# Kernel tuning notes

Hardware: AMD Instinct MI355X
Metric: run time of the kernel (lower is better)

The kernel has to match this reference:

```python
import jax, jax.numpy as jnp
import numpy as np

SEQ, BS, H, I, E = 2048, 4, 2048, 4096, 8


def setup_inputs() -> dict:
    key = jax.random.key(0)
    ks = jax.random.split(key, 5)
    s = 0.02
    return {
        "hidden_states": jax.random.normal(ks[0], (SEQ, BS, H), dtype=jnp.float32),
        "router_w": jax.random.normal(ks[1], (H, E), dtype=jnp.float32) * s,
        "gate_w": jax.random.normal(ks[2], (E, H, I), dtype=jnp.float32) * s,
        "up_w": jax.random.normal(ks[3], (E, H, I), dtype=jnp.float32) * s,
        "down_w": jax.random.normal(ks[4], (E, I, H), dtype=jnp.float32) * s,
    }


def reference(hidden_states, router_w, gate_w, up_w, down_w):
    # Router: [S,B,H] @ [H,E] -> [S,B,E]; top-1 routing (num_experts_per_tok == 1)
    router_logits = jnp.einsum("sbh,he->sbe", hidden_states, router_w)
    routing_indices = jnp.argmax(router_logits, axis=-1)  # [S,B]
    # sigmoid routing weights are computed but NOT applied in the original combine
    routing_weights = jax.nn.sigmoid(jnp.max(router_logits, axis=-1))  # noqa: F841

    out = jnp.zeros_like(hidden_states)
    for e in range(E):  # small fixed expert count
        mask = (routing_indices == e)[..., None]  # [S,B,1]
        g = jnp.einsum("sbh,hi->sbi", hidden_states, gate_w[e])
        u = jnp.einsum("sbh,hi->sbi", hidden_states, up_w[e])
        y = jnp.einsum("sbi,ih->sbh", jax.nn.silu(g) * u, down_w[e])
        out = out + jnp.where(mask, y, jnp.zeros((), out.dtype))
    return out
```

## Files before the change

kernel.cpp:

```cpp
#include <hip/hip_runtime.h>
#include <hip/hip_bf16.h>

#define T_TOKENS 8192
#define H_DIM 2048
#define I_DIM 4096
#define E_EXP 8
#define PAD_ROWS 9216

typedef __bf16 bf16x8 __attribute__((ext_vector_type(8)));
typedef float floatx4 __attribute__((ext_vector_type(4)));
typedef unsigned short ushort8 __attribute__((ext_vector_type(8)));

__device__ __forceinline__ unsigned short f2bf(float f) {
  union { float f; unsigned int i; } c; c.f = f;
  unsigned int x = c.i;
  unsigned int r = x + 0x7fffu + ((x >> 16) & 1u);
  return (unsigned short)(r >> 16);
}

__device__ __forceinline__ float bf2float(unsigned short u) {
  union { unsigned int i; float f; } c; c.i = ((unsigned int)u) << 16;
  return c.f;
}

__device__ __forceinline__ void gload_lds16(const void* g, void* l) {
  __builtin_amdgcn_global_load_lds(
      (const __attribute__((address_space(1))) void*)g,
      (__attribute__((address_space(3))) void*)l, 16, 0, 0);
}

__global__ __launch_bounds__(256) void xcvt_kernel(const float* __restrict__ x,
                                                   unsigned short* __restrict__ xb,
                                                   int* __restrict__ hdr) {
  if (blockIdx.x == 0 && threadIdx.x < 32) hdr[threadIdx.x] = 0;
  int i = (blockIdx.x * 256 + threadIdx.x) * 4;
  floatx4 v = *(const floatx4*)(x + i);
  unsigned short o0 = f2bf(v[0]), o1 = f2bf(v[1]), o2 = f2bf(v[2]), o3 = f2bf(v[3]);
  ushort4 o; o.x = o0; o.y = o1; o.z = o2; o.w = o3;
  *(ushort4*)(xb + i) = o;
}

__global__ __launch_bounds__(256) void router_kernel(const float* __restrict__ x,
                                                     const float* __restrict__ rw,
                                                     int* __restrict__ idx,
                                                     int* __restrict__ hdr) {
  int lane = threadIdx.x & 63;
  int t = blockIdx.x * 4 + (threadIdx.x >> 6);
  const float* xr = x + (size_t)t * H_DIM;
  float acc[8];
#pragma unroll
  for (int e = 0; e < 8; ++e) acc[e] = 0.f;
  for (int i = lane; i < H_DIM; i += 64) {
    float h = xr[i];
    floatx4 r0 = *(const floatx4*)(rw + i * 8);
    floatx4 r1 = *(const floatx4*)(rw + i * 8 + 4);
#pragma unroll
    for (int e = 0; e < 4; ++e) { acc[e] += h * r0[e]; acc[e + 4] += h * r1[e]; }
  }
#pragma unroll
  for (int off = 32; off > 0; off >>= 1)
#pragma unroll
    for (int e = 0; e < 8; ++e) acc[e] += __shfl_xor(acc[e], off, 64);
  if (lane == 0) {
    int best = 0; float bv = acc[0];
#pragma unroll
    for (int e = 1; e < 8; ++e) if (acc[e] > bv) { bv = acc[e]; best = e; }
    idx[t] = best;
    atomicAdd(&hdr[best], 1);
  }
}

__global__ __launch_bounds__(256) void setup_kernel(int* __restrict__ hdr,
                                                    int* __restrict__ rows) {
  if (threadIdx.x == 0) {
    int b = 0;
    for (int e = 0; e < 8; ++e) {
      hdr[16 + e] = b;
      b += ((hdr[e] + 127) >> 7) << 7;
    }
  }
  for (int i = threadIdx.x; i < PAD_ROWS; i += 256) rows[i] = -1;
}

__global__ __launch_bounds__(256) void scatter_kernel(const int* __restrict__ idx,
                                                      int* __restrict__ hdr,
                                                      int* __restrict__ rows) {
  int t = blockIdx.x * 256 + threadIdx.x;
  int e = idx[t];
  int p = atomicAdd(&hdr[8 + e], 1);
  rows[hdr[16 + e] + p] = t;
}

template <int K, int N>
__global__ __launch_bounds__(256) void wtrans_kernel(const float* __restrict__ W,
                                                     unsigned short* __restrict__ Wt) {
  __shared__ unsigned short tile[64 * 64];
  const int e = blockIdx.z;
  const int bn = blockIdx.x * 64;
  const int bk = blockIdx.y * 64;
  const float* Wp = W + (size_t)e * K * N;
  unsigned short* Wtp = Wt + (size_t)e * N * K;
  const int tid = threadIdx.x;

  {
    const int k = tid >> 2;
    const int n0 = (tid & 3) * 16;
    const float* src = Wp + (size_t)(bk + k) * N + bn + n0;
    floatx4 v0 = *(const floatx4*)(src);
    floatx4 v1 = *(const floatx4*)(src + 4);
    floatx4 v2 = *(const floatx4*)(src + 8);
    floatx4 v3 = *(const floatx4*)(src + 12);
    ushort8 p0, p1;
#pragma unroll
    for (int i = 0; i < 4; ++i) {
      p0[i] = f2bf(v0[i]); p0[4 + i] = f2bf(v1[i]);
      p1[i] = f2bf(v2[i]); p1[4 + i] = f2bf(v3[i]);
    }
    const int s0 = (tid & 3) * 2;
    *(ushort8*)(tile + k * 64 + ((s0 ^ (k & 7)) << 3)) = p0;
    *(ushort8*)(tile + k * 64 + (((s0 + 1) ^ (k & 7)) << 3)) = p1;
  }
  __syncthreads();
  {
    const int n = tid & 63;
    const int wv = tid >> 6;
    const int nhi = n >> 3, nlo = n & 7;
    ushort8 o0, o1;
#pragma unroll
    for (int i = 0; i < 8; ++i) {
      const int k0 = wv * 16 + i;
      const int k1 = k0 + 8;
      o0[i] = tile[k0 * 64 + (((nhi ^ (k0 & 7)) << 3) | nlo)];
      o1[i] = tile[k1 * 64 + (((nhi ^ (k1 & 7)) << 3) | nlo)];
    }
    unsigned short* dst = Wtp + (size_t)(bn + n) * K + bk + wv * 16;
    *(ushort8*)(dst) = o0;
    *(ushort8*)(dst + 8) = o1;
  }
}

template <int K, int NTOT, bool GATHER, int MODE>
__global__ __launch_bounds__(256) void moe_gemm(const unsigned short* __restrict__ A,
                                                const unsigned short* __restrict__ Bt,
                                                const int* __restrict__ hdr,
                                                const int* __restrict__ rows,
                                                unsigned short* __restrict__ gtmp,
                                                unsigned short* __restrict__ inter,
                                                float* __restrict__ outp) {
  const int e = blockIdx.z;
  const int cnt = hdr[e];
  if ((int)blockIdx.y * 128 >= cnt) return;
  const int seg = hdr[16 + e];

  const int tid = threadIdx.x;
  const int lane = tid & 63;
  const int wv = tid >> 6;
  const int wm = (wv & 1) * 64;
  const int wn = (wv >> 1) * 64;
  const int q = lane >> 4;
  const int l15 = lane & 15;

  __shared__ unsigned short sA[128 * 64];
  __shared__ unsigned short sB[128 * 64];

  const int lr = lane >> 3;
  const int colsw = (lane & 7) ^ lr;
  const unsigned short* aptr[4];
  const unsigned short* bptr[4];
  const unsigned short* Be = Bt + (size_t)e * NTOT * K;
#pragma unroll
  for (int j = 0; j < 4; ++j) {
    const int R = j * 32 + wv * 8 + lr;
    int ar;
    if (GATHER) {
      ar = rows[seg + blockIdx.y * 128 + R];
      if (ar < 0) ar = 0;
    } else {
      ar = seg + blockIdx.y * 128 + R;
    }
    aptr[j] = A + (size_t)ar * K + colsw * 8;
    bptr[j] = Be + (size_t)(blockIdx.x * 128 + R) * K + colsw * 8;
  }

  floatx4 acc[4][4];
#pragma unroll
  for (int a = 0; a < 4; ++a)
#pragma unroll
    for (int b = 0; b < 4; ++b) acc[a][b] = (floatx4){0.f, 0.f, 0.f, 0.f};

  for (int kt = 0; kt < K; kt += 64) {
#pragma unroll
    for (int j = 0; j < 4; ++j) {
      gload_lds16(aptr[j] + kt, sA + (j * 32 + wv * 8) * 64);
      gload_lds16(bptr[j] + kt, sB + (j * 32 + wv * 8) * 64);
    }
    __syncthreads();
#pragma unroll
    for (int ks = 0; ks < 64; ks += 32) {
      const int sbase = ks >> 3;
      bf16x8 af[4], bfr[4];
#pragma unroll
      for (int fm = 0; fm < 4; ++fm) {
        const int ra = wm + fm * 16 + l15;
        af[fm] = __builtin_bit_cast(bf16x8,
            *(const ushort8*)(sA + ra * 64 + (((q + sbase) ^ (ra & 7)) << 3)));
      }
#pragma unroll
      for (int fn = 0; fn < 4; ++fn) {
        const int rb = wn + fn * 16 + l15;
        bfr[fn] = __builtin_bit_cast(bf16x8,
            *(const ushort8*)(sB + rb * 64 + (((q + sbase) ^ (rb & 7)) << 3)));
      }
#pragma unroll
      for (int fm = 0; fm < 4; ++fm)
#pragma unroll
        for (int fn = 0; fn < 4; ++fn)
          acc[fm][fn] = __builtin_amdgcn_mfma_f32_16x16x32_bf16(af[fm], bfr[fn],
                                                                acc[fm][fn], 0, 0, 0);
    }
    __syncthreads();
  }

#pragma unroll
  for (int fm = 0; fm < 4; ++fm)
#pragma unroll
    for (int fn = 0; fn < 4; ++fn)
#pragma unroll
      for (int rr = 0; rr < 4; ++rr) {
        const int row = wm + fm * 16 + q * 4 + rr;
        const int col = wn + fn * 16 + l15;
        const int gm = blockIdx.y * 128 + row;
        const int gn = blockIdx.x * 128 + col;
        const float v = acc[fm][fn][rr];
        const size_t pos = (size_t)(seg + gm);
        if (MODE == 0) {
          gtmp[pos * NTOT + gn] = f2bf(v);
        } else if (MODE == 1) {
          const float g = bf2float(gtmp[pos * NTOT + gn]);
          const float s = g / (1.f + __expf(-g));
          inter[pos * NTOT + gn] = f2bf(s * v);
        } else {
          const int tok = rows[pos];
          if (tok >= 0) outp[(size_t)tok * NTOT + gn] = v;
        }
      }
}

extern "C" void kernel_launch(void* const* d_in, const int* in_sizes, int n_in,
                              void* d_out, int out_size, void* d_ws, size_t ws_size,
                              hipStream_t stream) {
  const float* hidden   = (const float*)d_in[0];
  const float* router_w = (const float*)d_in[1];
  const float* gate_w   = (const float*)d_in[2];
  const float* up_w     = (const float*)d_in[3];
  const float* down_w   = (const float*)d_in[4];
  float* out = (float*)d_out;

  char* ws = (char*)d_ws;
  int* hdr  = (int*)ws;
  int* idx  = (int*)(ws + 1024);
  int* rows = (int*)(ws + 33792);
  unsigned short* x_bf  = (unsigned short*)(ws + 70656);
  unsigned short* g_tmp = (unsigned short*)(ws + 33625088);
  unsigned short* W1    = (unsigned short*)(ws + 109122560);
  unsigned short* W2    = (unsigned short*)(ws + 243340288);
  unsigned short* inter = W1;
  unsigned short* downt = W2;

  xcvt_kernel<<<T_TOKENS * H_DIM / 1024, 256, 0, stream>>>(hidden, x_bf, hdr);
  router_kernel<<<T_TOKENS / 4, 256, 0, stream>>>(hidden, router_w, idx, hdr);
  setup_kernel<<<1, 256, 0, stream>>>(hdr, rows);
  scatter_kernel<<<T_TOKENS / 256, 256, 0, stream>>>(idx, hdr, rows);

  wtrans_kernel<H_DIM, I_DIM><<<dim3(I_DIM / 64, H_DIM / 64, E_EXP), 256, 0, stream>>>(gate_w, W1);
  wtrans_kernel<H_DIM, I_DIM><<<dim3(I_DIM / 64, H_DIM / 64, E_EXP), 256, 0, stream>>>(up_w, W2);

  moe_gemm<H_DIM, I_DIM, true, 0><<<dim3(I_DIM / 128, 64, E_EXP), 256, 0, stream>>>(
      x_bf, W1, hdr, rows, g_tmp, nullptr, nullptr);
  moe_gemm<H_DIM, I_DIM, true, 1><<<dim3(I_DIM / 128, 64, E_EXP), 256, 0, stream>>>(
      x_bf, W2, hdr, rows, g_tmp, inter, nullptr);

  wtrans_kernel<I_DIM, H_DIM><<<dim3(H_DIM / 64, I_DIM / 64, E_EXP), 256, 0, stream>>>(down_w, downt);
  moe_gemm<I_DIM, H_DIM, false, 2><<<dim3(H_DIM / 128, 64, E_EXP), 256, 0, stream>>>(
      inter, downt, hdr, rows, nullptr, nullptr, out);
}
```

Measured before the change: 1.684 ms.

## Fuse gate and up GEMMs into one kernel and rewrite weight transpose

Merges the gate and up projection GEMMs into a single kernel. It loads the gathered activation tile once, keeps two accumulator sets, and applies SiLU·up in the epilogue, so the bf16 gate intermediate no longer goes through memory. The weight transpose kernel now does register-only 8x8 transposes over 256-wide tiles instead of staging through LDS. Costs are higher register and LDS pressure in the fused kernel (launch_bounds 256,2), and the transpose writes are strided 16-byte stores.

```diff
diff --git a/kernel.cpp b/kernel.cpp
--- a/kernel.cpp
+++ b/kernel.cpp
@@ -94,59 +94,39 @@
 template <int K, int N>
 __global__ __launch_bounds__(256) void wtrans_kernel(const float* __restrict__ W,
                                                      unsigned short* __restrict__ Wt) {
-  __shared__ unsigned short tile[64 * 64];
   const int e = blockIdx.z;
-  const int bn = blockIdx.x * 64;
+  const int bn = blockIdx.x * 256;
   const int bk = blockIdx.y * 64;
   const float* Wp = W + (size_t)e * K * N;
   unsigned short* Wtp = Wt + (size_t)e * N * K;
   const int tid = threadIdx.x;
-
-  {
-    const int k = tid >> 2;
-    const int n0 = (tid & 3) * 16;
-    const float* src = Wp + (size_t)(bk + k) * N + bn + n0;
-    floatx4 v0 = *(const floatx4*)(src);
-    floatx4 v1 = *(const floatx4*)(src + 4);
-    floatx4 v2 = *(const floatx4*)(src + 8);
-    floatx4 v3 = *(const floatx4*)(src + 12);
-    ushort8 p0, p1;
-#pragma unroll
-    for (int i = 0; i < 4; ++i) {
-      p0[i] = f2bf(v0[i]); p0[4 + i] = f2bf(v1[i]);
-      p1[i] = f2bf(v2[i]); p1[4 + i] = f2bf(v3[i]);
-    }
-    const int s0 = (tid & 3) * 2;
-    *(ushort8*)(tile + k * 64 + ((s0 ^ (k & 7)) << 3)) = p0;
-    *(ushort8*)(tile + k * 64 + (((s0 + 1) ^ (k & 7)) << 3)) = p1;
-  }
-  __syncthreads();
-  {
-    const int n = tid & 63;
-    const int wv = tid >> 6;
-    const int nhi = n >> 3, nlo = n & 7;
-    ushort8 o0, o1;
-#pragma unroll
-    for (int i = 0; i < 8; ++i) {
-      const int k0 = wv * 16 + i;
-      const int k1 = k0 + 8;
-      o0[i] = tile[k0 * 64 + (((nhi ^ (k0 & 7)) << 3) | nlo)];
-      o1[i] = tile[k1 * 64 + (((nhi ^ (k1 & 7)) << 3) | nlo)];
-    }
-    unsigned short* dst = Wtp + (size_t)(bn + n) * K + bk + wv * 16;
-    *(ushort8*)(dst) = o0;
-    *(ushort8*)(dst + 8) = o1;
-  }
-}
-
-template <int K, int NTOT, bool GATHER, int MODE>
-__global__ __launch_bounds__(256) void moe_gemm(const unsigned short* __restrict__ A,
-                                                const unsigned short* __restrict__ Bt,
-                                                const int* __restrict__ hdr,
-                                                const int* __restrict__ rows,
-                                                unsigned short* __restrict__ gtmp,
-                                                unsigned short* __restrict__ inter,
-                                                float* __restrict__ outp) {
+  const int n0 = (tid & 31) * 8;
+  const int k0 = (tid >> 5) * 8;
+
+  const float* src = Wp + (size_t)(bk + k0) * N + bn + n0;
+  floatx4 a[8][2];
+#pragma unroll
+  for (int kk = 0; kk < 8; ++kk) {
+    a[kk][0] = *(const floatx4*)(src + (size_t)kk * N);
+    a[kk][1] = *(const floatx4*)(src + (size_t)kk * N + 4);
+  }
+  unsigned short* dst = Wtp + (size_t)(bn + n0) * K + bk + k0;
+#pragma unroll
+  for (int nn = 0; nn < 8; ++nn) {
+    ushort8 o;
+#pragma unroll
+    for (int kk = 0; kk < 8; ++kk) o[kk] = f2bf(a[kk][nn >> 2][nn & 3]);
+    *(ushort8*)(dst + (size_t)nn * K) = o;
+  }
+}
+
+__global__ __launch_bounds__(256, 2) void moe_gemm_gu(
+    const unsigned short* __restrict__ A,
+    const unsigned short* __restrict__ Bg,
+    const unsigned short* __restrict__ Bu,
+    const int* __restrict__ hdr,
+    const int* __restrict__ rows,
+    unsigned short* __restrict__ inter) {
   const int e = blockIdx.z;
   const int cnt = hdr[e];
   if ((int)blockIdx.y * 128 >= cnt) return;
@@ -161,38 +141,41 @@
   const int l15 = lane & 15;
 
   __shared__ unsigned short sA[128 * 64];
-  __shared__ unsigned short sB[128 * 64];
+  __shared__ unsigned short sBg[128 * 64];
+  __shared__ unsigned short sBu[128 * 64];
 
   const int lr = lane >> 3;
   const int colsw = (lane & 7) ^ lr;
   const unsigned short* aptr[4];
-  const unsigned short* bptr[4];
-  const unsigned short* Be = Bt + (size_t)e * NTOT * K;
+  const unsigned short* bgptr[4];
+  const unsigned short* buptr[4];
+  const unsigned short* BgE = Bg + (size_t)e * I_DIM * H_DIM;
+  const unsigned short* BuE = Bu + (size_t)e * I_DIM * H_DIM;
 #pragma unroll
   for (int j = 0; j < 4; ++j) {
     const int R = j * 32 + wv * 8 + lr;
-    int ar;
-    if (GATHER) {
-      ar = rows[seg + blockIdx.y * 128 + R];
-      if (ar < 0) ar = 0;
-    } else {
-      ar = seg + blockIdx.y * 128 + R;
-    }
-    aptr[j] = A + (size_t)ar * K + colsw * 8;
-    bptr[j] = Be + (size_t)(blockIdx.x * 128 + R) * K + colsw * 8;
-  }
-
-  floatx4 acc[4][4];
+    int ar = rows[seg + blockIdx.y * 128 + R];
+    if (ar < 0) ar = 0;
+    aptr[j] = A + (size_t)ar * H_DIM + colsw * 8;
+    bgptr[j] = BgE + (size_t)(blockIdx.x * 128 + R) * H_DIM + colsw * 8;
+    buptr[j] = BuE + (size_t)(blockIdx.x * 128 + R) * H_DIM + colsw * 8;
+  }
+
+  floatx4 accg[4][4], accu[4][4];
 #pragma unroll
   for (int a = 0; a < 4; ++a)
 #pragma unroll
-    for (int b = 0; b < 4; ++b) acc[a][b] = (floatx4){0.f, 0.f, 0.f, 0.f};
-
-  for (int kt = 0; kt < K; kt += 64) {
+    for (int b = 0; b < 4; ++b) {
+      accg[a][b] = (floatx4){0.f, 0.f, 0.f, 0.f};
+      accu[a][b] = (floatx4){0.f, 0.f, 0.f, 0.f};
+    }
+
+  for (int kt = 0; kt < H_DIM; kt += 64) {
 #pragma unroll
     for (int j = 0; j < 4; ++j) {
       gload_lds16(aptr[j] + kt, sA + (j * 32 + wv * 8) * 64);
-      gload_lds16(bptr[j] + kt, sB + (j * 32 + wv * 8) * 64);
+      gload_lds16(bgptr[j] + kt, sBg + (j * 32 + wv * 8) * 64);
+      gload_lds16(buptr[j] + kt, sBu + (j * 32 + wv * 8) * 64);
     }
     __syncthreads();
 #pragma unroll
@@ -209,14 +192,26 @@
       for (int fn = 0; fn < 4; ++fn) {
         const int rb = wn + fn * 16 + l15;
         bfr[fn] = __builtin_bit_cast(bf16x8,
-            *(const ushort8*)(sB + rb * 64 + (((q + sbase) ^ (rb & 7)) << 3)));
+            *(const ushort8*)(sBg + rb * 64 + (((q + sbase) ^ (rb & 7)) << 3)));
       }
 #pragma unroll
       for (int fm = 0; fm < 4; ++fm)
 #pragma unroll
         for (int fn = 0; fn < 4; ++fn)
-          acc[fm][fn] = __builtin_amdgcn_mfma_f32_16x16x32_bf16(af[fm], bfr[fn],
-                                                                acc[fm][fn], 0, 0, 0);
+          accg[fm][fn] = __builtin_amdgcn_mfma_f32_16x16x32_bf16(af[fm], bfr[fn],
+                                                                 accg[fm][fn], 0, 0, 0);
+#pragma unroll
+      for (int fn = 0; fn < 4; ++fn) {
+        const int rb = wn + fn * 16 + l15;
+        bfr[fn] = __builtin_bit_cast(bf16x8,
+            *(const ushort8*)(sBu + rb * 64 + (((q + sbase) ^ (rb & 7)) << 3)));
+      }
+#pragma unroll
+      for (int fm = 0; fm < 4; ++fm)
+#pragma unroll
+        for (int fn = 0; fn < 4; ++fn)
+          accu[fm][fn] = __builtin_amdgcn_mfma_f32_16x16x32_bf16(af[fm], bfr[fn],
+                                                                 accu[fm][fn], 0, 0, 0);
     }
     __syncthreads();
   }
@@ -231,18 +226,98 @@
         const int col = wn + fn * 16 + l15;
         const int gm = blockIdx.y * 128 + row;
         const int gn = blockIdx.x * 128 + col;
-        const float v = acc[fm][fn][rr];
-        const size_t pos = (size_t)(seg + gm);
-        if (MODE == 0) {
-          gtmp[pos * NTOT + gn] = f2bf(v);
-        } else if (MODE == 1) {
-          const float g = bf2float(gtmp[pos * NTOT + gn]);
-          const float s = g / (1.f + __expf(-g));
-          inter[pos * NTOT + gn] = f2bf(s * v);
-        } else {
-          const int tok = rows[pos];
-          if (tok >= 0) outp[(size_t)tok * NTOT + gn] = v;
-        }
+        const float g = accg[fm][fn][rr];
+        const float u = accu[fm][fn][rr];
+        const float s = g / (1.f + __expf(-g));
+        inter[(size_t)(seg + gm) * I_DIM + gn] = f2bf(s * u);
+      }
+}
+
+__global__ __launch_bounds__(256) void moe_gemm_down(
+    const unsigned short* __restrict__ A,
+    const unsigned short* __restrict__ Bt,
+    const int* __restrict__ hdr,
+    const int* __restrict__ rows,
+    float* __restrict__ outp) {
+  const int e = blockIdx.z;
+  const int cnt = hdr[e];
+  if ((int)blockIdx.y * 128 >= cnt) return;
+  const int seg = hdr[16 + e];
+
+  const int tid = threadIdx.x;
+  const int lane = tid & 63;
+  const int wv = tid >> 6;
+  const int wm = (wv & 1) * 64;
+  const int wn = (wv >> 1) * 64;
+  const int q = lane >> 4;
+  const int l15 = lane & 15;
+
+  __shared__ unsigned short sA[128 * 64];
+  __shared__ unsigned short sB[128 * 64];
+
+  const int lr = lane >> 3;
+  const int colsw = (lane & 7) ^ lr;
+  const unsigned short* aptr[4];
+  const unsigned short* bptr[4];
+  const unsigned short* Be = Bt + (size_t)e * H_DIM * I_DIM;
+#pragma unroll
+  for (int j = 0; j < 4; ++j) {
+    const int R = j * 32 + wv * 8 + lr;
+    aptr[j] = A + (size_t)(seg + blockIdx.y * 128 + R) * I_DIM + colsw * 8;
+    bptr[j] = Be + (size_t)(blockIdx.x * 128 + R) * I_DIM + colsw * 8;
+  }
+
+  floatx4 acc[4][4];
+#pragma unroll
+  for (int a = 0; a < 4; ++a)
+#pragma unroll
+    for (int b = 0; b < 4; ++b) acc[a][b] = (floatx4){0.f, 0.f, 0.f, 0.f};
+
+  for (int kt = 0; kt < I_DIM; kt += 64) {
+#pragma unroll
+    for (int j = 0; j < 4; ++j) {
+      gload_lds16(aptr[j] + kt, sA + (j * 32 + wv * 8) * 64);
+      gload_lds16(bptr[j] + kt, sB + (j * 32 + wv * 8) * 64);
+    }
+    __syncthreads();
+#pragma unroll
+    for (int ks = 0; ks < 64; ks += 32) {
+      const int sbase = ks >> 3;
+      bf16x8 af[4], bfr[4];
+#pragma unroll
+      for (int fm = 0; fm < 4; ++fm) {
+        const int ra = wm + fm * 16 + l15;
+        af[fm] = __builtin_bit_cast(bf16x8,
+            *(const ushort8*)(sA + ra * 64 + (((q + sbase) ^ (ra & 7)) << 3)));
+      }
+#pragma unroll
+      for (int fn = 0; fn < 4; ++fn) {
+        const int rb = wn + fn * 16 + l15;
+        bfr[fn] = __builtin_bit_cast(bf16x8,
+            *(const ushort8*)(sB + rb * 64 + (((q + sbase) ^ (rb & 7)) << 3)));
+      }
+#pragma unroll
+      for (int fm = 0; fm < 4; ++fm)
+#pragma unroll
+        for (int fn = 0; fn < 4; ++fn)
+          acc[fm][fn] = __builtin_amdgcn_mfma_f32_16x16x32_bf16(af[fm], bfr[fn],
+                                                                acc[fm][fn], 0, 0, 0);
+    }
+    __syncthreads();
+  }
+
+#pragma unroll
+  for (int fm = 0; fm < 4; ++fm)
+#pragma unroll
+    for (int fn = 0; fn < 4; ++fn)
+#pragma unroll
+      for (int rr = 0; rr < 4; ++rr) {
+        const int row = wm + fm * 16 + q * 4 + rr;
+        const int col = wn + fn * 16 + l15;
+        const int gm = blockIdx.y * 128 + row;
+        const int gn = blockIdx.x * 128 + col;
+        const int tok = rows[seg + gm];
+        if (tok >= 0) outp[(size_t)tok * H_DIM + gn] = acc[fm][fn][rr];
       }
 }
 
@@ -261,26 +336,23 @@
   int* idx  = (int*)(ws + 1024);
   int* rows = (int*)(ws + 33792);
   unsigned short* x_bf  = (unsigned short*)(ws + 70656);
-  unsigned short* g_tmp = (unsigned short*)(ws + 33625088);
+  unsigned short* inter = (unsigned short*)(ws + 33625088);
   unsigned short* W1    = (unsigned short*)(ws + 109122560);
   unsigned short* W2    = (unsigned short*)(ws + 243340288);
-  unsigned short* inter = W1;
-  unsigned short* downt = W2;
+  unsigned short* downt = W1;
 
   xcvt_kernel<<<T_TOKENS * H_DIM / 1024, 256, 0, stream>>>(hidden, x_bf, hdr);
   router_kernel<<<T_TOKENS / 4, 256, 0, stream>>>(hidden, router_w, idx, hdr);
   setup_kernel<<<1, 256, 0, stream>>>(hdr, rows);
   scatter_kernel<<<T_TOKENS / 256, 256, 0, stream>>>(idx, hdr, rows);
 
-  wtrans_kernel<H_DIM, I_DIM><<<dim3(I_DIM / 64, H_DIM / 64, E_EXP), 256, 0, stream>>>(gate_w, W1);
-  wtrans_kernel<H_DIM, I_DIM><<<dim3(I_DIM / 64, H_DIM / 64, E_EXP), 256, 0, stream>>>(up_w, W2);
-
-  moe_gemm<H_DIM, I_DIM, true, 0><<<dim3(I_DIM / 128, 64, E_EXP), 256, 0, stream>>>(
-      x_bf, W1, hdr, rows, g_tmp, nullptr, nullptr);
-  moe_gemm<H_DIM, I_DIM, true, 1><<<dim3(I_DIM / 128, 64, E_EXP), 256, 0, stream>>>(
-      x_bf, W2, hdr, rows, g_tmp, inter, nullptr);
-
-  wtrans_kernel<I_DIM, H_DIM><<<dim3(H_DIM / 64, I_DIM / 64, E_EXP), 256, 0, stream>>>(down_w, downt);
-  moe_gemm<I_DIM, H_DIM, false, 2><<<dim3(H_DIM / 128, 64, E_EXP), 256, 0, stream>>>(
-      inter, downt, hdr, rows, nullptr, nullptr, out);
-}
+  wtrans_kernel<H_DIM, I_DIM><<<dim3(I_DIM / 256, H_DIM / 64, E_EXP), 256, 0, stream>>>(gate_w, W1);
+  wtrans_kernel<H_DIM, I_DIM><<<dim3(I_DIM / 256, H_DIM / 64, E_EXP), 256, 0, stream>>>(up_w, W2);
+
+  moe_gemm_gu<<<dim3(I_DIM / 128, 64, E_EXP), 256, 0, stream>>>(
+      x_bf, W1, W2, hdr, rows, inter);
+
+  wtrans_kernel<I_DIM, H_DIM><<<dim3(H_DIM / 256, I_DIM / 64, E_EXP), 256, 0, stream>>>(down_w, downt);
+  moe_gemm_down<<<dim3(H_DIM / 128, 64, E_EXP), 256, 0, stream>>>(
+      inter, downt, hdr, rows, out);
+}
```

After: 1.549 ms. 1.09x faster.
